# Kernel tuning notes

Measured on AMD Instinct MI355X. Metric: run time of the kernel, lower is better.

## Reference

```python
import jax, jax.numpy as jnp
import numpy as np


def setup_inputs() -> dict:
    key = jax.random.key(0)
    ks = jax.random.split(key, 12)
    N, T, V, C, O, IC, S = 32, 256, 25, 64, 64, 16, 3
    rn = lambda k, sh, s=1.0: jax.random.normal(k, sh, dtype=jnp.float32) * s
    return {
        "x": rn(ks[0], (N, T, V, C)),
        "A": jax.random.uniform(ks[1], (S, V, V), dtype=jnp.float32),
        "PA": rn(ks[2], (S, V, V), 0.01),
        "weight_A": jax.random.uniform(ks[3], (4,), dtype=jnp.float32),
        "Wa": rn(ks[4], (S, C, IC), 1.0 / np.sqrt(C)),
        "ba": rn(ks[5], (S, IC), 0.01),
        "Wb": rn(ks[6], (S, C, IC), 1.0 / np.sqrt(C)),
        "bb": rn(ks[7], (S, IC), 0.01),
        "Wd": rn(ks[8], (S, C, O), 1.0 / np.sqrt(C)),
        "bd": rn(ks[9], (S, O), 0.01),
        "gamma": jax.random.uniform(ks[10], (O,), dtype=jnp.float32),
        "beta": rn(ks[11], (O,), 0.1),
    }


def reference(x, A, PA, weight_A, Wa, ba, Wb, bb, Wd, bd, gamma, beta):
    # unit_gcn_confirm forward (in_channels == out_channels, so `down` = identity)
    N, T, V, C = x.shape
    S, _, IC = Wa.shape
    BN_EPS = 1e-5

    # A = w0 * A_static + w1 * softmax(PA)  -> (S, V, V)
    A_comb = weight_A[0] * A + weight_A[1] * jax.nn.softmax(PA, axis=-1)

    # per-subset Q/K projections: (S, N, T, V, IC)
    qa = jnp.einsum('ntvc,sci->sntvi', x, Wa) + ba[:, None, None, None, :]
    kb = jnp.einsum('ntvc,sci->sntvi', x, Wb) + bb[:, None, None, None, :]

    # A1: time-flattened attention over nodes, scale sqrt(IC*T) -> (S, N, V, V)
    A1 = jax.nn.softmax(
        jnp.einsum('sntui,sntvi->snuv', qa, kb) / jnp.sqrt(jnp.float32(IC * T)),
        axis=-1)
    # A2: per-frame attention over nodes, scale sqrt(IC) -> (S, N, T, V, V)
    A2 = jax.nn.softmax(
        jnp.einsum('sntui,sntvi->sntuv', qa, kb) / jnp.sqrt(jnp.float32(IC)),
        axis=-1)

    # combined adjacency per subset: (S, N, T, V, V)
    A_in = (A_comb[:, None, None, :, :]
            + weight_A[2] * A1[:, :, None, :, :]
            + weight_A[3] * A2)

    # message passing + per-subset output linear, summed over subsets
    z = jnp.einsum('sntuv,ntvc->sntuc', A_in, x)             # (S, N, T, V, C)
    y = jnp.einsum('sntuc,sco->ntuo', z, Wd) + bd.sum(0)     # (N, T, V, O)

    # BatchNorm2d in inference mode (running_mean=0, running_var=1)
    y = y * (gamma / jnp.sqrt(1.0 + BN_EPS)) + beta

    # residual (down = identity since in_channels == out_channels) + relu
    return jax.nn.relu(y + x)
```

## Files before the change

kernel.cpp:

```cpp
#include <hip/hip_runtime.h>
#include <hip/hip_bf16.h>

typedef __hip_bfloat16 bf16;
typedef __attribute__((ext_vector_type(8))) short short8;
typedef __attribute__((ext_vector_type(4))) float f32x4;

#define S  3
#define V  25
#define C  64
#define O  64
#define IC 16
#define NN 32
#define TT 256
#define TB 4
#define TCH 8

__device__ __forceinline__ float b2f(bf16 v) { return __bfloat162float(v); }

__device__ __forceinline__ float ldv(const void* p, size_t i, int f32) {
    return f32 ? ((const float*)p)[i] : b2f(((const bf16*)p)[i]);
}

__device__ __forceinline__ unsigned short f2bf(float f) {
    bf16 h = __float2bfloat16(f);
    return *(unsigned short*)&h;
}

__global__ __launch_bounds__(256) void k_prep(
    const void* __restrict__ x,
    const void* __restrict__ A, const void* __restrict__ PA,
    const void* __restrict__ wA,
    const void* __restrict__ Wa, const void* __restrict__ Wb,
    const void* __restrict__ Wd,
    float* __restrict__ A_comb, float* __restrict__ S1,
    unsigned short* __restrict__ wprep, int* __restrict__ flagp) {
    __shared__ int sflag;
    if (threadIdx.x < 64) {
        const bf16* p = (const bf16*)x;
        int bad = 0;
        #pragma unroll
        for (int k = 0; k < 32; k++) {
            float v = b2f(p[threadIdx.x + k * 64]);
            bad |= !(v > -1000.f && v < 1000.f);
        }
        unsigned long long m = __ballot(bad);
        if (threadIdx.x == 0) {
            sflag = (m != 0ull) ? 1 : 0;
            if (blockIdx.x == 0) *flagp = sflag;
        }
    }
    __syncthreads();
    int f32 = sflag;

    int g = blockIdx.x * 256 + threadIdx.x;
    int stride = gridDim.x * 256;

    for (int w = g; w < 60000; w += stride) S1[w] = 0.f;

    for (int w = g; w < 3456; w += stride) {
        int s = w / 1152, r = w % 1152, i = r / 72, c = r % 72;
        unsigned short va = 0, vb = 0;
        if (c < 64) {
            va = f2bf(ldv(Wa, (size_t)s * 1024 + c * 16 + i, f32));
            vb = f2bf(ldv(Wb, (size_t)s * 1024 + c * 16 + i, f32));
        }
        wprep[s * 6912 + i * 72 + c] = va;
        wprep[s * 6912 + 1152 + i * 72 + c] = vb;
    }
    for (int w = g; w < 13824; w += stride) {
        int s = w / 4608, r = w % 4608, o = r / 72, c = r % 72;
        unsigned short vd = 0;
        if (c < 64) vd = f2bf(ldv(Wd, (size_t)s * 4096 + c * 64 + o, f32));
        wprep[s * 6912 + 2304 + o * 72 + c] = vd;
    }

    if (g < S * V) {
        float w0 = ldv(wA, 0, f32), w1 = ldv(wA, 1, f32);
        float vals[V];
        float m = -1e30f;
        for (int v = 0; v < V; v++) { vals[v] = ldv(PA, g * V + v, f32); m = fmaxf(m, vals[v]); }
        float sum = 0.f;
        for (int v = 0; v < V; v++) { vals[v] = __expf(vals[v] - m); sum += vals[v]; }
        float inv = 1.f / sum;
        for (int v = 0; v < V; v++)
            A_comb[g * V + v] = w0 * ldv(A, g * V + v, f32) + w1 * vals[v] * inv;
    }
}

#define P1_QK(sidx, QB, KB) do {                                              \
    const unsigned short* wat_ = wprep + (size_t)(sidx) * 6912;               \
    const unsigned short* wbt_ = wat_ + 1152;                                 \
    short8 wa0 = *(const short8*)&wat_[lm * 72 + kq * 8];                     \
    short8 wa1 = *(const short8*)&wat_[lm * 72 + 32 + kq * 8];                \
    short8 wb0 = *(const short8*)&wbt_[lm * 72 + kq * 8];                     \
    short8 wb1 = *(const short8*)&wbt_[lm * 72 + 32 + kq * 8];                \
    f32x4 q = __builtin_amdgcn_mfma_f32_16x16x32_bf16(xa0, wa0, (f32x4){0.f,0.f,0.f,0.f}, 0, 0, 0); \
    q = __builtin_amdgcn_mfma_f32_16x16x32_bf16(xa1, wa1, q, 0, 0, 0);        \
    f32x4 k = __builtin_amdgcn_mfma_f32_16x16x32_bf16(xa0, wb0, (f32x4){0.f,0.f,0.f,0.f}, 0, 0, 0); \
    k = __builtin_amdgcn_mfma_f32_16x16x32_bf16(xa1, wb1, k, 0, 0, 0);        \
    _Pragma("unroll")                                                         \
    for (int reg = 0; reg < 4; reg++) {                                       \
        (QB)[(drow0 + reg) * 20 + lm] = f2bf(q[reg] + rbq[sidx]);             \
        (KB)[(drow0 + reg) * 20 + lm] = f2bf(k[reg] + rbk[sidx]);             \
    }                                                                         \
} while (0)

#define E_ACC(AC, QB, KB) do {                                                \
    short8 a_ = *(const short8*)&(QB)[(tsel + ur0 + lm) * 20 + ksel];         \
    short8 b_ = *(const short8*)&(KB)[(tsel + vc0 + lm) * 20 + ksel];         \
    (AC) = __builtin_amdgcn_mfma_f32_16x16x32_bf16(a_, b_, (AC), 0, 0, 0);    \
} while (0)

#define STAGE_XB(TTOFF) do {                                                  \
    if (f32) {                                                                \
        const float4* xp = (const float4*)x + (size_t)(n * TT + t0 + (TTOFF)) * 400; \
        for (int w = tid; w < 800; w += 256) {                                \
            int t = w / 400, r = w % 400, u = r >> 4, c4 = r & 15;            \
            float4 v = xp[w];                                                 \
            unsigned short h[4] = {f2bf(v.x), f2bf(v.y), f2bf(v.z), f2bf(v.w)}; \
            *(uint2*)&xb[(t * 32 + u) * 72 + c4 * 4] = *(uint2*)h;            \
        }                                                                     \
    } else {                                                                  \
        const unsigned int* xp = (const unsigned int*)x;                      \
        size_t base2 = (size_t)(n * TT + t0 + (TTOFF)) * V * C / 2;           \
        for (int w = tid; w < 1600; w += 256) {                               \
            int t = w / 800, r = w % 800, u = r >> 5, c2 = r & 31;            \
            ((unsigned int*)xb)[(t * 32 + u) * 36 + c2] = xp[base2 + (size_t)(t * V + u) * 32 + c2]; \
        }                                                                     \
    }                                                                         \
} while (0)

__global__ __launch_bounds__(256) void k_s1(
    const void* __restrict__ x,
    const unsigned short* __restrict__ wprep,
    const void* __restrict__ ba, const void* __restrict__ bb,
    float* __restrict__ S1g, const int* __restrict__ flagp) {
    int f32 = *flagp;
    int tchunk = blockIdx.x, n = blockIdx.y;
    int tid = threadIdx.x;
    int lane = tid & 63, wv = tid >> 6;
    int lm = lane & 15, kq = lane >> 4;

    __shared__ __align__(16) unsigned short xb[64 * 72];
    __shared__ __align__(16) unsigned short qb[3][64 * 20];
    __shared__ __align__(16) unsigned short kb_[3][64 * 20];

    float rbq[3], rbk[3];
    #pragma unroll
    for (int s = 0; s < 3; s++) {
        rbq[s] = ldv(ba, s * IC + lm, f32);
        rbk[s] = ldv(bb, s * IC + lm, f32);
    }

    int mrow = wv * 16 + lm;
    int drow0 = wv * 16 + (kq << 2);
    int ur0 = ((wv >> 1) & 1) << 4;
    int vc0 = (wv & 1) << 4;
    int t0 = tchunk * TCH;
    int tsel = (kq >> 1) << 5;
    int ksel = (kq & 1) << 3;

    f32x4 acc0 = {0.f,0.f,0.f,0.f}, acc1 = {0.f,0.f,0.f,0.f}, acc2 = {0.f,0.f,0.f,0.f};

    STAGE_XB(0);
    __syncthreads();

    for (int pp = 0; pp < TCH / 2; pp++) {
        short8 xa0 = *(const short8*)&xb[mrow * 72 + kq * 8];
        short8 xa1 = *(const short8*)&xb[mrow * 72 + 32 + kq * 8];
        P1_QK(0, qb[0], kb_[0]);
        P1_QK(1, qb[1], kb_[1]);
        P1_QK(2, qb[2], kb_[2]);
        __syncthreads();
        E_ACC(acc0, qb[0], kb_[0]);
        E_ACC(acc1, qb[1], kb_[1]);
        E_ACC(acc2, qb[2], kb_[2]);
        if (pp < TCH / 2 - 1) STAGE_XB(2 * pp + 2);
        __syncthreads();
    }

    {
        int u = ur0 + (kq << 2), v = vc0 + lm;
        float* d0 = S1g + (size_t)n * 625;
        float* d1 = S1g + ((size_t)NN + n) * 625;
        float* d2 = S1g + ((size_t)2 * NN + n) * 625;
        #pragma unroll
        for (int reg = 0; reg < 4; reg++) {
            if (u + reg < V && v < V) {
                atomicAdd(&d0[(u + reg) * 25 + v], acc0[reg]);
                atomicAdd(&d1[(u + reg) * 25 + v], acc1[reg]);
                atomicAdd(&d2[(u + reg) * 25 + v], acc2[reg]);
            }
        }
    }
}

__global__ void k_a1(float* __restrict__ S1g, const float* __restrict__ A_comb,
                     const void* __restrict__ wA, const int* __restrict__ flagp) {
    int f32 = *flagp;
    float w2 = ldv(wA, 2, f32);
    int sn = blockIdx.x;
    int s = sn / NN;
    int u = threadIdx.x;
    if (u >= V) return;
    float* row = S1g + (size_t)sn * V * V + u * V;
    const float* ac = A_comb + (size_t)(s * V + u) * V;
    const float scale = 1.0f / 64.0f;
    float vals[V];
    float m = -1e30f;
    for (int v = 0; v < V; v++) { vals[v] = row[v] * scale; m = fmaxf(m, vals[v]); }
    float sum = 0.f;
    for (int v = 0; v < V; v++) { vals[v] = __expf(vals[v] - m); sum += vals[v]; }
    float inv = w2 / sum;
    for (int v = 0; v < V; v++) row[v] = ac[v] + vals[v] * inv;
}

#define SM_HALF(EA, EB, UH) do {                                              \
    _Pragma("unroll")                                                         \
    for (int reg = 0; reg < 4; reg++) {                                       \
        float p0 = __expf((EA)[reg] * 0.25f);                                 \
        float p1 = (lm < V - 16) ? __expf((EB)[reg] * 0.25f) : 0.f;           \
        float pr = p0 + p1;                                                   \
        pr += __shfl_xor(pr, 1);                                              \
        pr += __shfl_xor(pr, 2);                                              \
        pr += __shfl_xor(pr, 4);                                              \
        pr += __shfl_xor(pr, 8);                                              \
        float si = w3 / pr;                                                   \
        int u = (UH) * 16 + (kq << 2) + reg;                                  \
        float a0v = (u < V) ? (pa0[UH][reg] + si * p0) : 0.f;                 \
        float a1v = (u < V && lm < V - 16) ? (pa1[UH][reg] + si * p1) : 0.f;  \
        qab[(wv * 32 + (UH) * 16 + (kq << 2) + reg) * 40 + lm] = f2bf(a0v);   \
        qab[(wv * 32 + (UH) * 16 + (kq << 2) + reg) * 40 + 16 + lm] = f2bf(a1v); \
    }                                                                         \
} while (0)

__global__ __launch_bounds__(256, 3) void k_main(
    const void* __restrict__ x,
    const void* __restrict__ ba, const void* __restrict__ bb,
    const void* __restrict__ bd,
    const void* __restrict__ gamma, const void* __restrict__ beta,
    const void* __restrict__ wA,
    const unsigned short* __restrict__ wprep,
    const float* __restrict__ ac1g,
    void* __restrict__ outp, const int* __restrict__ flagp) {
    int f32 = *flagp;
    int bx = blockIdx.x;
    int n = bx >> 6, tc = bx & 63;
    int t0 = tc * TB;
    int tid = threadIdx.x;
    int lane = tid & 63, wv = tid >> 6;
    int lm = lane & 15, kq = lane >> 4;

    __shared__ __align__(16) unsigned short pool[22016];
    unsigned short* xb  = pool;
    unsigned short* qab = pool + 9216;
    unsigned short* kbb = pool + 14336;
    unsigned short* xws = pool + 19456 + wv * 640;

    if (f32) {
        const float4* xp = (const float4*)x + (size_t)(n * TT + t0) * 400;
        for (int w = tid; w < 1600; w += 256) {
            int t = w / 400, r = w % 400, u = r >> 4, c4 = r & 15;
            float4 v = xp[w];
            unsigned short h[4] = {f2bf(v.x), f2bf(v.y), f2bf(v.z), f2bf(v.w)};
            *(uint2*)&xb[(t * 32 + u) * 72 + c4 * 4] = *(uint2*)h;
        }
    } else {
        const unsigned int* xp = (const unsigned int*)x;
        size_t base2 = (size_t)(n * TT + t0) * V * C / 2;
        for (int w = tid; w < 3200; w += 256) {
            int t = w / 800, r = w % 800, u = r >> 5, c2 = r & 31;
            ((unsigned int*)xb)[(t * 32 + u) * 36 + c2] = xp[base2 + (size_t)(t * V + u) * 32 + c2];
        }
    }
    for (int w = tid; w < 28 * 36; w += 256) {
        int idx = w / 36, word = w % 36;
        int t = idx / 7, ur = 25 + idx % 7;
        ((unsigned int*)xb)[(t * 32 + ur) * 36 + word] = 0;
    }
    for (int w = tid; w < 1024; w += 256) {
        int r = w >> 3, cw = 8 + (w & 7);
        ((unsigned int*)qab)[r * 20 + cw] = 0;
        ((unsigned int*)kbb)[r * 20 + cw] = 0;
    }
    float w3 = ldv(wA, 3, f32);

    f32x4 acc0[4], acc1[4];
    #pragma unroll
    for (int nt = 0; nt < 4; nt++) {
        acc0[nt] = (f32x4){0.f, 0.f, 0.f, 0.f};
        acc1[nt] = (f32x4){0.f, 0.f, 0.f, 0.f};
    }

    __syncthreads();

    short8 xa00 = *(const short8*)&xb[(wv * 32 + lm) * 72 + kq * 8];
    short8 xa01 = *(const short8*)&xb[(wv * 32 + lm) * 72 + 32 + kq * 8];
    short8 xa10 = *(const short8*)&xb[(wv * 32 + 16 + lm) * 72 + kq * 8];
    short8 xa11 = *(const short8*)&xb[(wv * 32 + 16 + lm) * 72 + 32 + kq * 8];

    for (int s = 0; s < S; s++) {
        const unsigned short* watg = wprep + s * 6912;
        const unsigned short* wbtg = watg + 1152;
        const unsigned short* wdtg = watg + 2304;
        const float* acn = ac1g + ((size_t)s * NN + n) * 625;
        float bq_c = ldv(ba, s * IC + lm, f32);
        float bk_c = ldv(bb, s * IC + lm, f32);

        {
            short8 wa0 = *(const short8*)&watg[lm * 72 + kq * 8];
            short8 wa1 = *(const short8*)&watg[lm * 72 + 32 + kq * 8];
            short8 wb0 = *(const short8*)&wbtg[lm * 72 + kq * 8];
            short8 wb1 = *(const short8*)&wbtg[lm * 72 + 32 + kq * 8];
            f32x4 q0 = __builtin_amdgcn_mfma_f32_16x16x32_bf16(xa00, wa0, (f32x4){0.f,0.f,0.f,0.f}, 0, 0, 0);
            q0 = __builtin_amdgcn_mfma_f32_16x16x32_bf16(xa01, wa1, q0, 0, 0, 0);
            f32x4 q1 = __builtin_amdgcn_mfma_f32_16x16x32_bf16(xa10, wa0, (f32x4){0.f,0.f,0.f,0.f}, 0, 0, 0);
            q1 = __builtin_amdgcn_mfma_f32_16x16x32_bf16(xa11, wa1, q1, 0, 0, 0);
            f32x4 k0 = __builtin_amdgcn_mfma_f32_16x16x32_bf16(xa00, wb0, (f32x4){0.f,0.f,0.f,0.f}, 0, 0, 0);
            k0 = __builtin_amdgcn_mfma_f32_16x16x32_bf16(xa01, wb1, k0, 0, 0, 0);
            f32x4 k1 = __builtin_amdgcn_mfma_f32_16x16x32_bf16(xa10, wb0, (f32x4){0.f,0.f,0.f,0.f}, 0, 0, 0);
            k1 = __builtin_amdgcn_mfma_f32_16x16x32_bf16(xa11, wb1, k1, 0, 0, 0);
            int r0 = wv * 32 + (kq << 2);
            #pragma unroll
            for (int reg = 0; reg < 4; reg++) {
                qab[(r0 + reg) * 40 + lm]      = f2bf(q0[reg] + bq_c);
                qab[(r0 + 16 + reg) * 40 + lm] = f2bf(q1[reg] + bq_c);
                kbb[(r0 + reg) * 40 + lm]      = f2bf(k0[reg] + bk_c);
                kbb[(r0 + 16 + reg) * 40 + lm] = f2bf(k1[reg] + bk_c);
            }
        }

        float pa0[2][4], pa1[2][4];
        #pragma unroll
        for (int uh = 0; uh < 2; uh++)
            #pragma unroll
            for (int reg = 0; reg < 4; reg++) {
                int u = uh * 16 + (kq << 2) + reg;
                int uc = (u < V) ? u : 0;
                pa0[uh][reg] = acn[uc * 25 + lm];
                pa1[uh][reg] = (lm < V - 16) ? acn[uc * 25 + 16 + lm] : 0.f;
            }

        {
            short8 aq0 = *(const short8*)&qab[(wv * 32 + lm) * 40 + kq * 8];
            short8 aq1 = *(const short8*)&qab[(wv * 32 + 16 + lm) * 40 + kq * 8];
            short8 bk0 = *(const short8*)&kbb[(wv * 32 + lm) * 40 + kq * 8];
            short8 bk1 = *(const short8*)&kbb[(wv * 32 + 16 + lm) * 40 + kq * 8];
            f32x4 e00 = __builtin_amdgcn_mfma_f32_16x16x32_bf16(aq0, bk0, (f32x4){0.f,0.f,0.f,0.f}, 0, 0, 0);
            f32x4 e01 = __builtin_amdgcn_mfma_f32_16x16x32_bf16(aq0, bk1, (f32x4){0.f,0.f,0.f,0.f}, 0, 0, 0);
            f32x4 e10 = __builtin_amdgcn_mfma_f32_16x16x32_bf16(aq1, bk0, (f32x4){0.f,0.f,0.f,0.f}, 0, 0, 0);
            f32x4 e11 = __builtin_amdgcn_mfma_f32_16x16x32_bf16(aq1, bk1, (f32x4){0.f,0.f,0.f,0.f}, 0, 0, 0);
            SM_HALF(e00, e01, 0);
            SM_HALF(e10, e11, 1);
        }

        {
            short8 aA0 = *(const short8*)&qab[(wv * 32 + lm) * 40 + kq * 8];
            short8 aA1 = *(const short8*)&qab[(wv * 32 + 16 + lm) * 40 + kq * 8];
            #pragma unroll
            for (int nt = 0; nt < 4; nt++) {
                short8 wd0 = *(const short8*)&wdtg[(nt * 16 + lm) * 72 + kq * 8];
                short8 wd1 = *(const short8*)&wdtg[(nt * 16 + lm) * 72 + 32 + kq * 8];
                f32x4 xw0 = __builtin_amdgcn_mfma_f32_16x16x32_bf16(xa00, wd0, (f32x4){0.f,0.f,0.f,0.f}, 0, 0, 0);
                xw0 = __builtin_amdgcn_mfma_f32_16x16x32_bf16(xa01, wd1, xw0, 0, 0, 0);
                f32x4 xw1 = __builtin_amdgcn_mfma_f32_16x16x32_bf16(xa10, wd0, (f32x4){0.f,0.f,0.f,0.f}, 0, 0, 0);
                xw1 = __builtin_amdgcn_mfma_f32_16x16x32_bf16(xa11, wd1, xw1, 0, 0, 0);
                unsigned short h0[4] = {f2bf(xw0[0]), f2bf(xw0[1]), f2bf(xw0[2]), f2bf(xw0[3])};
                unsigned short h1[4] = {f2bf(xw1[0]), f2bf(xw1[1]), f2bf(xw1[2]), f2bf(xw1[3])};
                *(uint2*)&xws[lm * 40 + (kq << 2)]      = *(uint2*)h0;
                *(uint2*)&xws[lm * 40 + 16 + (kq << 2)] = *(uint2*)h1;
                short8 bx8 = *(const short8*)&xws[lm * 40 + kq * 8];
                acc0[nt] = __builtin_amdgcn_mfma_f32_16x16x32_bf16(aA0, bx8, acc0[nt], 0, 0, 0);
                acc1[nt] = __builtin_amdgcn_mfma_f32_16x16x32_bf16(aA1, bx8, acc1[nt], 0, 0, 0);
            }
        }
        if (s < S - 1) {
            #pragma unroll
            for (int reg = 0; reg < 4; reg++) {
                qab[(wv * 32 + (kq << 2) + reg) * 40 + 16 + lm] = 0;
                qab[(wv * 32 + 16 + (kq << 2) + reg) * 40 + 16 + lm] = 0;
            }
        }
    }

    __syncthreads();

    if (f32) {
        #pragma unroll
        for (int nt = 0; nt < 4; nt++) {
            int o = nt * 16 + lm;
            float g = ldv(gamma, o, 1) * rsqrtf(1.f + 1e-5f);
            float bt_ = ldv(beta, o, 1);
            float bsum = ldv(bd, o, 1) + ldv(bd, O + o, 1) + ldv(bd, 2 * O + o, 1);
            #pragma unroll
            for (int uh = 0; uh < 2; uh++)
                #pragma unroll
                for (int reg = 0; reg < 4; reg++) {
                    int u = uh * 16 + (kq << 2) + reg;
                    if (u < V) {
                        float av = uh ? acc1[nt][reg] : acc0[nt][reg];
                        float xres = b2f(*(const bf16*)&xb[(wv * 32 + u) * 72 + o]);
                        float yv = fmaxf((av + bsum) * g + bt_ + xres, 0.f);
                        size_t ob = (size_t)((n * TT + t0 + wv) * V + u) * O + o;
                        ((float*)outp)[ob] = yv;
                    }
                }
        }
    } else {
        unsigned short* ep = pool + 9216;
        #pragma unroll
        for (int nt = 0; nt < 4; nt++) {
            int o = nt * 16 + lm;
            float g = ldv(gamma, o, 0) * rsqrtf(1.f + 1e-5f);
            float bt_ = ldv(beta, o, 0);
            float bsum = ldv(bd, o, 0) + ldv(bd, O + o, 0) + ldv(bd, 2 * O + o, 0);
            #pragma unroll
            for (int uh = 0; uh < 2; uh++)
                #pragma unroll
                for (int reg = 0; reg < 4; reg++) {
                    int u = uh * 16 + (kq << 2) + reg;
                    if (u < V) {
                        float av = uh ? acc1[nt][reg] : acc0[nt][reg];
                        float xres = b2f(*(const bf16*)&xb[(wv * 32 + u) * 72 + o]);
                        float yv = fmaxf((av + bsum) * g + bt_ + xres, 0.f);
                        ep[(wv * V + u) * O + o] = f2bf(yv);
                    }
                }
        }
        __syncthreads();
        uint4* outv = (uint4*)((bf16*)outp + (size_t)(n * TT + t0) * V * O);
        const uint4* epv = (const uint4*)ep;
        for (int w = tid; w < 800; w += 256) outv[w] = epv[w];
    }
}

extern "C" void kernel_launch(void* const* d_in, const int* in_sizes, int n_in,
                              void* d_out, int out_size, void* d_ws, size_t ws_size,
                              hipStream_t stream) {
    const void* x     = d_in[0];
    const void* A     = d_in[1];
    const void* PA    = d_in[2];
    const void* wA    = d_in[3];
    const void* Wa    = d_in[4];
    const void* ba    = d_in[5];
    const void* Wb    = d_in[6];
    const void* bb    = d_in[7];
    const void* Wd    = d_in[8];
    const void* bd    = d_in[9];
    const void* gamma = d_in[10];
    const void* beta  = d_in[11];

    int*   flagp  = (int*)d_ws;
    float* wsf    = (float*)d_ws;
    float* A_comb = wsf + 64;
    float* S1     = wsf + 2048;
    unsigned short* wprep = (unsigned short*)(wsf + 65536);

    k_prep<<<256, 256, 0, stream>>>(x, A, PA, wA, Wa, Wb, Wd, A_comb, S1, wprep, flagp);
    k_s1<<<dim3(TT / TCH, NN), 256, 0, stream>>>(x, wprep, ba, bb, S1, flagp);
    k_a1<<<S * NN, 64, 0, stream>>>(S1, A_comb, wA, flagp);
    k_main<<<NN * TT / TB, 256, 0, stream>>>(x, ba, bb, bd, gamma, beta, wA,
                                             wprep, S1, d_out, flagp);
}
```

Measured before the change: 190.7 us.

## Restructure S1 kernel: per-wave frame pairs in registers, LDS reduction before global atomics

```diff
diff --git a/kernel.cpp b/kernel.cpp
--- a/kernel.cpp
+++ b/kernel.cpp
@@ -87,50 +87,7 @@
     }
 }
 
-#define P1_QK(sidx, QB, KB) do {                                              \
-    const unsigned short* wat_ = wprep + (size_t)(sidx) * 6912;               \
-    const unsigned short* wbt_ = wat_ + 1152;                                 \
-    short8 wa0 = *(const short8*)&wat_[lm * 72 + kq * 8];                     \
-    short8 wa1 = *(const short8*)&wat_[lm * 72 + 32 + kq * 8];                \
-    short8 wb0 = *(const short8*)&wbt_[lm * 72 + kq * 8];                     \
-    short8 wb1 = *(const short8*)&wbt_[lm * 72 + 32 + kq * 8];                \
-    f32x4 q = __builtin_amdgcn_mfma_f32_16x16x32_bf16(xa0, wa0, (f32x4){0.f,0.f,0.f,0.f}, 0, 0, 0); \
-    q = __builtin_amdgcn_mfma_f32_16x16x32_bf16(xa1, wa1, q, 0, 0, 0);        \
-    f32x4 k = __builtin_amdgcn_mfma_f32_16x16x32_bf16(xa0, wb0, (f32x4){0.f,0.f,0.f,0.f}, 0, 0, 0); \
-    k = __builtin_amdgcn_mfma_f32_16x16x32_bf16(xa1, wb1, k, 0, 0, 0);        \
-    _Pragma("unroll")                                                         \
-    for (int reg = 0; reg < 4; reg++) {                                       \
-        (QB)[(drow0 + reg) * 20 + lm] = f2bf(q[reg] + rbq[sidx]);             \
-        (KB)[(drow0 + reg) * 20 + lm] = f2bf(k[reg] + rbk[sidx]);             \
-    }                                                                         \
-} while (0)
-
-#define E_ACC(AC, QB, KB) do {                                                \
-    short8 a_ = *(const short8*)&(QB)[(tsel + ur0 + lm) * 20 + ksel];         \
-    short8 b_ = *(const short8*)&(KB)[(tsel + vc0 + lm) * 20 + ksel];         \
-    (AC) = __builtin_amdgcn_mfma_f32_16x16x32_bf16(a_, b_, (AC), 0, 0, 0);    \
-} while (0)
-
-#define STAGE_XB(TTOFF) do {                                                  \
-    if (f32) {                                                                \
-        const float4* xp = (const float4*)x + (size_t)(n * TT + t0 + (TTOFF)) * 400; \
-        for (int w = tid; w < 800; w += 256) {                                \
-            int t = w / 400, r = w % 400, u = r >> 4, c4 = r & 15;            \
-            float4 v = xp[w];                                                 \
-            unsigned short h[4] = {f2bf(v.x), f2bf(v.y), f2bf(v.z), f2bf(v.w)}; \
-            *(uint2*)&xb[(t * 32 + u) * 72 + c4 * 4] = *(uint2*)h;            \
-        }                                                                     \
-    } else {                                                                  \
-        const unsigned int* xp = (const unsigned int*)x;                      \
-        size_t base2 = (size_t)(n * TT + t0 + (TTOFF)) * V * C / 2;           \
-        for (int w = tid; w < 1600; w += 256) {                               \
-            int t = w / 800, r = w % 800, u = r >> 5, c2 = r & 31;            \
-            ((unsigned int*)xb)[(t * 32 + u) * 36 + c2] = xp[base2 + (size_t)(t * V + u) * 32 + c2]; \
-        }                                                                     \
-    }                                                                         \
-} while (0)
-
-__global__ __launch_bounds__(256) void k_s1(
+__global__ __launch_bounds__(256, 3) void k_s1(
     const void* __restrict__ x,
     const unsigned short* __restrict__ wprep,
     const void* __restrict__ ba, const void* __restrict__ bb,
@@ -141,9 +98,13 @@
     int lane = tid & 63, wv = tid >> 6;
     int lm = lane & 15, kq = lane >> 4;
 
-    __shared__ __align__(16) unsigned short xb[64 * 72];
-    __shared__ __align__(16) unsigned short qb[3][64 * 20];
-    __shared__ __align__(16) unsigned short kb_[3][64 * 20];
+    __shared__ __align__(16) unsigned short qb[4][1280];
+    __shared__ __align__(16) unsigned short kb_[4][1280];
+    __shared__ __align__(16) float s1t[S * 625];
+    unsigned short* qbw = qb[wv];
+    unsigned short* kbw = kb_[wv];
+
+    for (int w = tid; w < S * 625; w += 256) s1t[w] = 0.f;
 
     float rbq[3], rbk[3];
     #pragma unroll
@@ -152,46 +113,90 @@
         rbk[s] = ldv(bb, s * IC + lm, f32);
     }
 
-    int mrow = wv * 16 + lm;
-    int drow0 = wv * 16 + (kq << 2);
-    int ur0 = ((wv >> 1) & 1) << 4;
-    int vc0 = (wv & 1) << 4;
-    int t0 = tchunk * TCH;
+    int tA = tchunk * TCH + 2 * wv;
+
+    short8 xf[8];
+    #pragma unroll
+    for (int rg = 0; rg < 4; rg++) {
+        int th = rg >> 1, uh = rg & 1;
+        int u = uh * 16 + lm;
+        bool ok = (u < V);
+        size_t rbase = ((size_t)(n * TT + tA + th) * V + (ok ? u : 0)) * C;
+        #pragma unroll
+        for (int hf = 0; hf < 2; hf++) {
+            short8 v8 = {0, 0, 0, 0, 0, 0, 0, 0};
+            if (ok) {
+                if (f32) {
+                    const float* xr = (const float*)x + rbase + hf * 32 + kq * 8;
+                    float4 a = *(const float4*)xr;
+                    float4 b = *(const float4*)(xr + 4);
+                    unsigned short h[8] = {f2bf(a.x), f2bf(a.y), f2bf(a.z), f2bf(a.w),
+                                           f2bf(b.x), f2bf(b.y), f2bf(b.z), f2bf(b.w)};
+                    v8 = *(short8*)h;
+                } else {
+                    v8 = *(const short8*)((const bf16*)x + rbase + hf * 32 + kq * 8);
+                }
+            }
+            xf[rg * 2 + hf] = v8;
+        }
+    }
+
+    __syncthreads();
+
+    f32x4 acc[3][4];
+    #pragma unroll
+    for (int s = 0; s < 3; s++)
+        #pragma unroll
+        for (int qd = 0; qd < 4; qd++)
+            acc[s][qd] = (f32x4){0.f, 0.f, 0.f, 0.f};
+
     int tsel = (kq >> 1) << 5;
     int ksel = (kq & 1) << 3;
 
-    f32x4 acc0 = {0.f,0.f,0.f,0.f}, acc1 = {0.f,0.f,0.f,0.f}, acc2 = {0.f,0.f,0.f,0.f};
-
-    STAGE_XB(0);
+    #pragma unroll
+    for (int s = 0; s < S; s++) {
+        const unsigned short* wat_ = wprep + (size_t)s * 6912;
+        const unsigned short* wbt_ = wat_ + 1152;
+        short8 wa0 = *(const short8*)&wat_[lm * 72 + kq * 8];
+        short8 wa1 = *(const short8*)&wat_[lm * 72 + 32 + kq * 8];
+        short8 wb0 = *(const short8*)&wbt_[lm * 72 + kq * 8];
+        short8 wb1 = *(const short8*)&wbt_[lm * 72 + 32 + kq * 8];
+        #pragma unroll
+        for (int rg = 0; rg < 4; rg++) {
+            f32x4 q = __builtin_amdgcn_mfma_f32_16x16x32_bf16(xf[rg * 2], wa0, (f32x4){0.f,0.f,0.f,0.f}, 0, 0, 0);
+            q = __builtin_amdgcn_mfma_f32_16x16x32_bf16(xf[rg * 2 + 1], wa1, q, 0, 0, 0);
+            f32x4 k = __builtin_amdgcn_mfma_f32_16x16x32_bf16(xf[rg * 2], wb0, (f32x4){0.f,0.f,0.f,0.f}, 0, 0, 0);
+            k = __builtin_amdgcn_mfma_f32_16x16x32_bf16(xf[rg * 2 + 1], wb1, k, 0, 0, 0);
+            #pragma unroll
+            for (int reg = 0; reg < 4; reg++) {
+                qbw[(rg * 16 + (kq << 2) + reg) * 20 + lm] = f2bf(q[reg] + rbq[s]);
+                kbw[(rg * 16 + (kq << 2) + reg) * 20 + lm] = f2bf(k[reg] + rbk[s]);
+            }
+        }
+        #pragma unroll
+        for (int qd = 0; qd < 4; qd++) {
+            int ur0 = (qd >> 1) << 4, vc0 = (qd & 1) << 4;
+            short8 a_ = *(const short8*)&qbw[(tsel + ur0 + lm) * 20 + ksel];
+            short8 b_ = *(const short8*)&kbw[(tsel + vc0 + lm) * 20 + ksel];
+            acc[s][qd] = __builtin_amdgcn_mfma_f32_16x16x32_bf16(a_, b_, acc[s][qd], 0, 0, 0);
+        }
+    }
+
+    #pragma unroll
+    for (int s = 0; s < S; s++)
+        #pragma unroll
+        for (int qd = 0; qd < 4; qd++) {
+            int u0 = (qd >> 1) * 16 + (kq << 2), v = (qd & 1) * 16 + lm;
+            #pragma unroll
+            for (int reg = 0; reg < 4; reg++)
+                if (u0 + reg < V && v < V)
+                    atomicAdd(&s1t[s * 625 + (u0 + reg) * 25 + v], acc[s][qd][reg]);
+        }
     __syncthreads();
 
-    for (int pp = 0; pp < TCH / 2; pp++) {
-        short8 xa0 = *(const short8*)&xb[mrow * 72 + kq * 8];
-        short8 xa1 = *(const short8*)&xb[mrow * 72 + 32 + kq * 8];
-        P1_QK(0, qb[0], kb_[0]);
-        P1_QK(1, qb[1], kb_[1]);
-        P1_QK(2, qb[2], kb_[2]);
-        __syncthreads();
-        E_ACC(acc0, qb[0], kb_[0]);
-        E_ACC(acc1, qb[1], kb_[1]);
-        E_ACC(acc2, qb[2], kb_[2]);
-        if (pp < TCH / 2 - 1) STAGE_XB(2 * pp + 2);
-        __syncthreads();
-    }
-
-    {
-        int u = ur0 + (kq << 2), v = vc0 + lm;
-        float* d0 = S1g + (size_t)n * 625;
-        float* d1 = S1g + ((size_t)NN + n) * 625;
-        float* d2 = S1g + ((size_t)2 * NN + n) * 625;
-        #pragma unroll
-        for (int reg = 0; reg < 4; reg++) {
-            if (u + reg < V && v < V) {
-                atomicAdd(&d0[(u + reg) * 25 + v], acc0[reg]);
-                atomicAdd(&d1[(u + reg) * 25 + v], acc1[reg]);
-                atomicAdd(&d2[(u + reg) * 25 + v], acc2[reg]);
-            }
-        }
+    for (int w = tid; w < S * 625; w += 256) {
+        int s = w / 625, r = w % 625;
+        atomicAdd(&S1g[((size_t)s * NN + n) * 625 + r], s1t[w]);
     }
 }
 
```

Measured after the change: 219.9 us. 15.3% more time.
